# Performance work log

Measured on AMD Instinct MI355X. Metric: run time of the kernel, lower is better.

Reference implementation:

```python
import jax, jax.numpy as jnp
import numpy as np

N_HEAD = 12

def setup_inputs() -> dict:
    key = jax.random.key(0)
    k1, k2, k3 = jax.random.split(key, 3)
    B, T, C = 1, 4096, 768
    x = jax.random.normal(k1, (B, T, C), dtype=jnp.float32)
    w_attn = jax.random.normal(k2, (C, 3 * C), dtype=jnp.float32) * 0.02
    w_proj = jax.random.normal(k3, (C, C), dtype=jnp.float32) * 0.02
    return {"x": x, "w_attn": w_attn, "w_proj": w_proj}

def reference(x, w_attn, w_proj):
    B, T, C = x.shape
    H = N_HEAD
    hd = C // H
    scale = 1.0 / jnp.sqrt(jnp.asarray(hd, dtype=x.dtype))
    qkv = x @ w_attn  # [B,T,3C]
    q, k, v = jnp.split(qkv, 3, axis=-1)
    # [B,T,C] -> [B,H,T,hd]
    q = q.reshape(B, T, H, hd).transpose(0, 2, 1, 3)
    k = k.reshape(B, T, H, hd).transpose(0, 2, 1, 3)
    v = v.reshape(B, T, H, hd).transpose(0, 2, 1, 3)
    att = jnp.einsum("bhqd,bhkd->bhqk", q, k) * scale  # [B,H,T,T]
    causal = jnp.tril(jnp.ones((T, T), dtype=bool))
    att = jnp.where(causal[None, None], att, -jnp.inf)
    att = jax.nn.softmax(att, axis=-1)
    y = jnp.einsum("bhqk,bhkd->bhqd", att, v)  # [B,H,T,hd]
    y = y.transpose(0, 2, 1, 3).reshape(B, T, C)
    return y @ w_proj
```

## Files before the change

### kernel.cpp

```cpp
#include <hip/hip_runtime.h>
#include <hip/hip_bf16.h>

typedef __attribute__((ext_vector_type(8))) short bfx8;
typedef __attribute__((ext_vector_type(4))) short bfx4;
typedef __attribute__((ext_vector_type(4))) float f32x4;
typedef __attribute__((ext_vector_type(4))) unsigned int u32x4;
typedef __attribute__((ext_vector_type(2))) unsigned int u32x2;

#define T_SEQ 4096
#define C_DIM 768
#define NH    12
#define HD    64
#define QKV_N 2304
#define QK_N  1536

#define MFMA16(a, b, c) __builtin_amdgcn_mfma_f32_16x16x32_bf16((a), (b), (c), 0, 0, 0)

#if __has_builtin(__builtin_amdgcn_exp2f)
#define EXP2(x) __builtin_amdgcn_exp2f(x)
#else
#define EXP2(x) exp2f(x)
#endif

__device__ __forceinline__ short f2bf(float f) {
  __hip_bfloat16 h = __float2bfloat16(f);
  return __builtin_bit_cast(short, h);
}

__device__ __forceinline__ void pl16(unsigned& a, unsigned& b) {
#if __has_builtin(__builtin_amdgcn_permlane16_swap)
  u32x2 r = __builtin_amdgcn_permlane16_swap(a, b, false, false);
  a = r[0]; b = r[1];
#else
  unsigned ax = (unsigned)__shfl_xor((int)a, 16, 64);
  unsigned bx = (unsigned)__shfl_xor((int)b, 16, 64);
  bool odd = ((threadIdx.x >> 4) & 1) != 0;
  unsigned na = odd ? bx : a;
  unsigned nb = odd ? b : ax;
  a = na; b = nb;
#endif
}
__device__ __forceinline__ void pl32(unsigned& a, unsigned& b) {
#if __has_builtin(__builtin_amdgcn_permlane32_swap)
  u32x2 r = __builtin_amdgcn_permlane32_swap(a, b, false, false);
  a = r[0]; b = r[1];
#else
  unsigned ax = (unsigned)__shfl_xor((int)a, 32, 64);
  unsigned bx = (unsigned)__shfl_xor((int)b, 32, 64);
  bool hi = ((threadIdx.x >> 5) & 1) != 0;
  unsigned na = hi ? bx : a;
  unsigned nb = hi ? b : ax;
  a = na; b = nb;
#endif
}

__global__ __launch_bounds__(256) void conv_bf16_kernel(
    const float* __restrict__ in, short* __restrict__ out, int n4) {
  int i = blockIdx.x * 256 + threadIdx.x;
  if (i >= n4) return;
  float4 v = ((const float4*)in)[i];
  bfx4 o;
  o[0] = f2bf(v.x); o[1] = f2bf(v.y); o[2] = f2bf(v.z); o[3] = f2bf(v.w);
  ((bfx4*)out)[i] = o;
}

__global__ __launch_bounds__(256) void transpose_bf16_kernel(
    const float* __restrict__ in, short* __restrict__ out, int R, int Cc,
    int qcols, float qscale) {
  __shared__ short tile[32][33];
  int bx = blockIdx.x * 32, by = blockIdx.y * 32;
  int tx = threadIdx.x & 31, ty = threadIdx.x >> 5;
  float sc = (bx + tx) < qcols ? qscale : 1.0f;
#pragma unroll
  for (int i = 0; i < 32; i += 8)
    tile[ty + i][tx] = f2bf(in[(size_t)(by + ty + i) * Cc + (bx + tx)] * sc);
  __syncthreads();
#pragma unroll
  for (int i = 0; i < 32; i += 8)
    out[(size_t)(bx + ty + i) * R + (by + tx)] = tile[tx][ty + i];
}

template <int MODE>
__global__ __launch_bounds__(256) void gemm_bf16(
    const short* __restrict__ A, const short* __restrict__ Bt,
    void* __restrict__ Cout, short* __restrict__ Vt,
    int M, int N, int K) {
  __shared__ short As[2][128 * 32];
  __shared__ short Bs[2][128 * 32];
  const int tid  = threadIdx.x;
  const int lane = tid & 63;
  const int wave = tid >> 6;
  const int am0 = blockIdx.x * 128;
  const int bn0 = blockIdx.y * 128;
  const int wr = (wave >> 1) * 64;
  const int wc = (wave & 1) * 64;

  const int idx0 = tid,       r0 = idx0 >> 2, c0 = (idx0 & 3) * 8;
  const int idx1 = 256 + tid, r1 = idx1 >> 2, c1 = (idx1 & 3) * 8;

#define GSTAGE(buf, k0)                                                                 \
  do {                                                                                  \
    __builtin_amdgcn_global_load_lds(                                                   \
        (const __attribute__((address_space(1))) void*)(A + (size_t)(am0 + r0) * K + (k0) + c0), \
        (__attribute__((address_space(3))) void*)(&As[buf][idx0 * 8]), 16, 0, 0);       \
    __builtin_amdgcn_global_load_lds(                                                   \
        (const __attribute__((address_space(1))) void*)(A + (size_t)(am0 + r1) * K + (k0) + c1), \
        (__attribute__((address_space(3))) void*)(&As[buf][idx1 * 8]), 16, 0, 0);       \
    __builtin_amdgcn_global_load_lds(                                                   \
        (const __attribute__((address_space(1))) void*)(Bt + (size_t)(bn0 + r0) * K + (k0) + c0), \
        (__attribute__((address_space(3))) void*)(&Bs[buf][idx0 * 8]), 16, 0, 0);       \
    __builtin_amdgcn_global_load_lds(                                                   \
        (const __attribute__((address_space(1))) void*)(Bt + (size_t)(bn0 + r1) * K + (k0) + c1), \
        (__attribute__((address_space(3))) void*)(&Bs[buf][idx1 * 8]), 16, 0, 0);       \
  } while (0)

  const f32x4 zero = {0.f, 0.f, 0.f, 0.f};
  f32x4 acc[4][4];
#pragma unroll
  for (int i = 0; i < 4; i++)
#pragma unroll
    for (int j = 0; j < 4; j++) acc[i][j] = zero;

  const int aoff = (wr + (lane & 15)) * 32 + (lane >> 4) * 8;
  const int boff = (wc + (lane & 15)) * 32 + (lane >> 4) * 8;

  const int nk = K / 32;
  GSTAGE(0, 0);
  for (int t = 0; t < nk; t++) {
    const int cur = t & 1;
    if (t + 1 < nk) {
      GSTAGE(cur ^ 1, (t + 1) * 32);
      asm volatile("s_waitcnt vmcnt(4)" ::: "memory");
    } else {
      asm volatile("s_waitcnt vmcnt(0)" ::: "memory");
    }
    __builtin_amdgcn_s_barrier();

    bfx8 a[4], b[4];
#pragma unroll
    for (int mf = 0; mf < 4; mf++)
      a[mf] = *(const bfx8*)&As[cur][aoff + mf * 16 * 32];
#pragma unroll
    for (int nf = 0; nf < 4; nf++)
      b[nf] = *(const bfx8*)&Bs[cur][boff + nf * 16 * 32];
#pragma unroll
    for (int mf = 0; mf < 4; mf++)
#pragma unroll
      for (int nf = 0; nf < 4; nf++)
        acc[mf][nf] = MFMA16(a[mf], b[nf], acc[mf][nf]);

    asm volatile("s_waitcnt lgkmcnt(0)" ::: "memory");
    __builtin_amdgcn_s_barrier();
  }
#undef GSTAGE

  if (MODE == 1 && bn0 >= QK_N) {
#pragma unroll
    for (int mf = 0; mf < 4; mf++) {
      int row0 = am0 + wr + mf * 16 + (lane >> 4) * 4;
#pragma unroll
      for (int nf = 0; nf < 4; nf++) {
        int colV = bn0 - QK_N + wc + nf * 16 + (lane & 15);
        bfx4 ov;
#pragma unroll
        for (int r = 0; r < 4; r++) ov[r] = f2bf(acc[mf][nf][r]);
        *(bfx4*)&Vt[(size_t)colV * T_SEQ + row0] = ov;
      }
    }
  } else {
#pragma unroll
    for (int mf = 0; mf < 4; mf++) {
#pragma unroll
      for (int r = 0; r < 4; r++) {
        int row = am0 + wr + mf * 16 + (lane >> 4) * 4 + r;
#pragma unroll
        for (int nf = 0; nf < 4; nf++) {
          int col = bn0 + wc + nf * 16 + (lane & 15);
          float v = acc[mf][nf][r];
          if (MODE == 1)
            ((short*)Cout)[(size_t)row * QK_N + col] = f2bf(v);
          else
            ((float*)Cout)[(size_t)row * N + col] = v;
        }
      }
    }
  }
}

__global__ __launch_bounds__(256) void attn_kernel(
    const short* __restrict__ qk, const short* __restrict__ Vt,
    short* __restrict__ yb) {
  __shared__ short Ks[2][64 * 64];
  __shared__ short Vs[2][64 * 64];

  const int tid  = threadIdx.x;
  const int lane = tid & 63;
  const int wv   = tid >> 6;
  const int col  = lane & 15;
  const int g    = lane >> 4;

  const int bid = blockIdx.x;
  const int h   = bid % NH;
  const int pr  = bid / NH;
  const int myi = (wv < 2) ? (127 - pr) : pr;
  const int qw  = myi * 32 + (wv & 1) * 16;
  const int nt  = ((127 - pr) * 32 + 31) / 64 + 1;

  const int hq = h * HD;
  const int hk = C_DIM + h * HD;
  const short* Vth = Vt + (size_t)h * HD * T_SEQ;

  const int sidx0 = tid;
  const int sidx1 = 256 + tid;
  const int srow0 = sidx0 >> 3, sslot0 = (sidx0 & 7) ^ (srow0 & 7);
  const int srow1 = sidx1 >> 3, sslot1 = (sidx1 & 7) ^ (srow1 & 7);

#define STAGE(buf, kvoff)                                                               \
  do {                                                                                  \
    __builtin_amdgcn_global_load_lds(                                                   \
        (const __attribute__((address_space(1))) void*)(qk + (size_t)((kvoff) + srow0) * QK_N + hk + sslot0 * 8), \
        (__attribute__((address_space(3))) void*)(&Ks[buf][sidx0 * 8]), 16, 0, 0);      \
    __builtin_amdgcn_global_load_lds(                                                   \
        (const __attribute__((address_space(1))) void*)(qk + (size_t)((kvoff) + srow1) * QK_N + hk + sslot1 * 8), \
        (__attribute__((address_space(3))) void*)(&Ks[buf][sidx1 * 8]), 16, 0, 0);      \
    __builtin_amdgcn_global_load_lds(                                                   \
        (const __attribute__((address_space(1))) void*)(Vth + (size_t)srow0 * T_SEQ + (kvoff) + sslot0 * 8), \
        (__attribute__((address_space(3))) void*)(&Vs[buf][sidx0 * 8]), 16, 0, 0);      \
    __builtin_amdgcn_global_load_lds(                                                   \
        (const __attribute__((address_space(1))) void*)(Vth + (size_t)srow1 * T_SEQ + (kvoff) + sslot1 * 8), \
        (__attribute__((address_space(3))) void*)(&Vs[buf][sidx1 * 8]), 16, 0, 0);      \
  } while (0)

  bfx8 qf[2];
#pragma unroll
  for (int hf = 0; hf < 2; hf++)
    qf[hf] = *(const bfx8*)&qk[(size_t)(qw + col) * QK_N + hq + hf * 32 + g * 8];

  int koff[4][2], voff[2][4];
#pragma unroll
  for (int sub = 0; sub < 4; sub++) {
    int row = sub * 16 + col;
#pragma unroll
    for (int hf = 0; hf < 2; hf++)
      koff[sub][hf] = row * 64 + ((((hf << 2) | g) ^ (row & 7)) * 8);
  }
#pragma unroll
  for (int ks = 0; ks < 2; ks++)
#pragma unroll
    for (int c = 0; c < 4; c++) {
      int row = c * 16 + col;
      voff[ks][c] = row * 64 + ((((ks << 2) | g) ^ (row & 7)) * 8);
    }

  bfx8 ones;
#pragma unroll
  for (int j = 0; j < 8; j++) ones[j] = (short)0x3F80;

  const f32x4 zero = {0.f, 0.f, 0.f, 0.f};
  f32x4 o[4];
#pragma unroll
  for (int c = 0; c < 4; c++) o[c] = zero;
  f32x4 o_l = zero;

  const int qabs = qw + col;

#define TILE_BODY(BUF, KV)                                                              \
  do {                                                                                  \
    if ((KV) <= qw + 15) {                                                              \
      bfx8 kf[4][2];                                                                    \
      _Pragma("unroll") for (int sub = 0; sub < 4; sub++)                               \
          _Pragma("unroll") for (int hf = 0; hf < 2; hf++)                              \
              kf[sub][hf] = *(const bfx8*)&Ks[BUF][koff[sub][hf]];                      \
      bfx8 vtf[2][4];                                                                   \
      _Pragma("unroll") for (int ks = 0; ks < 2; ks++)                                  \
          _Pragma("unroll") for (int c = 0; c < 4; c++)                                 \
              vtf[ks][c] = *(const bfx8*)&Vs[BUF][voff[ks][c]];                         \
      f32x4 s[4];                                                                       \
      __builtin_amdgcn_s_setprio(1);                                                    \
      _Pragma("unroll") for (int sub = 0; sub < 4; sub++) {                             \
        s[sub] = zero;                                                                  \
        s[sub] = MFMA16(kf[sub][0], qf[0], s[sub]);                                     \
        s[sub] = MFMA16(kf[sub][1], qf[1], s[sub]);                                     \
      }                                                                                 \
      __builtin_amdgcn_s_setprio(0);                                                    \
      if (!((KV) + 63 <= qw)) {                                                         \
        _Pragma("unroll") for (int sub = 0; sub < 4; sub++)                             \
            _Pragma("unroll") for (int r = 0; r < 4; r++) {                             \
              int key = (KV) + sub * 16 + 4 * g + r;                                    \
              if (key > qabs) s[sub][r] = -INFINITY;                                    \
            }                                                                           \
      }                                                                                 \
      unsigned u[4][4];                                                                 \
      _Pragma("unroll") for (int sub = 0; sub < 4; sub++)                               \
          _Pragma("unroll") for (int r = 0; r < 4; r++) {                               \
            float pv = EXP2(s[sub][r]);                                                 \
            u[sub][r] = __builtin_bit_cast(unsigned, pv) & 0xFFFF0000u;                 \
          }                                                                             \
      _Pragma("unroll") for (int ks = 0; ks < 2; ks++) {                                \
        unsigned x0 = u[2 * ks][1] | (u[2 * ks][0] >> 16);                              \
        unsigned y0 = u[2 * ks + 1][1] | (u[2 * ks + 1][0] >> 16);                      \
        unsigned x1 = u[2 * ks][3] | (u[2 * ks][2] >> 16);                              \
        unsigned y1 = u[2 * ks + 1][3] | (u[2 * ks + 1][2] >> 16);                      \
        pl32(x0, y0); pl16(x0, y0);                                                     \
        pl32(x1, y1); pl16(x1, y1);                                                     \
        u32x4 w; w[0] = x0; w[1] = x1; w[2] = y0; w[3] = y1;                            \
        bfx8 pf = __builtin_bit_cast(bfx8, w);                                          \
        __builtin_amdgcn_s_setprio(1);                                                  \
        _Pragma("unroll") for (int c = 0; c < 4; c++)                                   \
            o[c] = MFMA16(vtf[ks][c], pf, o[c]);                                        \
        o_l = MFMA16(ones, pf, o_l);                                                    \
        __builtin_amdgcn_s_setprio(0);                                                  \
      }                                                                                 \
    }                                                                                   \
  } while (0)

  STAGE(0, 0);

  int t = 0;
  while (true) {
    if (t + 1 < nt) {
      STAGE(1, (t + 1) * 64);
      asm volatile("s_waitcnt vmcnt(4)" ::: "memory");
    } else {
      asm volatile("s_waitcnt vmcnt(0)" ::: "memory");
    }
    __builtin_amdgcn_s_barrier();
    TILE_BODY(0, t * 64);
    asm volatile("s_waitcnt lgkmcnt(0)" ::: "memory");
    __builtin_amdgcn_s_barrier();
    if (++t >= nt) break;

    if (t + 1 < nt) {
      STAGE(0, (t + 1) * 64);
      asm volatile("s_waitcnt vmcnt(4)" ::: "memory");
    } else {
      asm volatile("s_waitcnt vmcnt(0)" ::: "memory");
    }
    __builtin_amdgcn_s_barrier();
    TILE_BODY(1, t * 64);
    asm volatile("s_waitcnt lgkmcnt(0)" ::: "memory");
    __builtin_amdgcn_s_barrier();
    if (++t >= nt) break;
  }

  float inv = 1.f / o_l[0];
#pragma unroll
  for (int c = 0; c < 4; c++) {
    bfx4 ov;
#pragma unroll
    for (int r = 0; r < 4; r++) ov[r] = f2bf(o[c][r] * inv);
    *(bfx4*)&yb[(size_t)(qw + col) * C_DIM + h * HD + c * 16 + g * 4] = ov;
  }
#undef TILE_BODY
#undef STAGE
}

extern "C" void kernel_launch(void* const* d_in, const int* in_sizes, int n_in,
                              void* d_out, int out_size, void* d_ws, size_t ws_size,
                              hipStream_t stream) {
  const float* x      = (const float*)d_in[0];
  const float* w_attn = (const float*)d_in[1];
  const float* w_proj = (const float*)d_in[2];
  float* out = (float*)d_out;

  char* ws = (char*)d_ws;
  short* xb  = (short*)(ws);
  short* wab = (short*)(ws + 6291456);
  short* wpb = (short*)(ws + 9830400);
  short* qk  = (short*)(ws + 11010048);
  short* Vt  = (short*)(ws + 23592960);
  short* yb  = (short*)(ws + 29884416);

  conv_bf16_kernel<<<3072, 256, 0, stream>>>(x, xb, 786432);
  transpose_bf16_kernel<<<dim3(QKV_N / 32, C_DIM / 32), 256, 0, stream>>>(
      w_attn, wab, C_DIM, QKV_N, C_DIM, 0.125f * 1.4426950408889634f);
  transpose_bf16_kernel<<<dim3(C_DIM / 32, C_DIM / 32), 256, 0, stream>>>(
      w_proj, wpb, C_DIM, C_DIM, 0, 1.0f);

  gemm_bf16<1><<<dim3(T_SEQ / 128, QKV_N / 128), 256, 0, stream>>>(
      xb, wab, (void*)qk, Vt, T_SEQ, QKV_N, C_DIM);
  attn_kernel<<<64 * NH, 256, 0, stream>>>(qk, Vt, yb);
  gemm_bf16<0><<<dim3(T_SEQ / 128, C_DIM / 128), 256, 0, stream>>>(
      yb, wpb, (void*)out, nullptr, T_SEQ, C_DIM, C_DIM);
}
```

Baseline: 122.2 us.

## Process two 16-row query groups per wave in attention, halving block threads

The attention block drops from four waves to two, and each wave now handles 32 query rows (two 16-row groups) instead of 16. The K/V fragments read from LDS are reused across both groups, which halves LDS read traffic per query. Staging is redistributed so 128 threads issue four loads each. The probability packing also switches to a byte-permute helper. The cost is higher register pressure and fewer waves per block to hide latency, so occupancy or latency hiding may suffer.

```diff
diff --git a/kernel.cpp b/kernel.cpp
--- a/kernel.cpp
+++ b/kernel.cpp
@@ -25,6 +25,16 @@
 __device__ __forceinline__ short f2bf(float f) {
   __hip_bfloat16 h = __float2bfloat16(f);
   return __builtin_bit_cast(short, h);
+}
+
+__device__ __forceinline__ unsigned packtrunc(float p_even, float p_odd) {
+#if __has_builtin(__builtin_amdgcn_perm)
+  return __builtin_amdgcn_perm(__builtin_bit_cast(unsigned, p_odd),
+                               __builtin_bit_cast(unsigned, p_even), 0x07060302u);
+#else
+  return (__builtin_bit_cast(unsigned, p_odd) & 0xFFFF0000u) |
+         (__builtin_bit_cast(unsigned, p_even) >> 16);
+#endif
 }
 
 __device__ __forceinline__ void pl16(unsigned& a, unsigned& b) {
@@ -187,7 +197,7 @@
   }
 }
 
-__global__ __launch_bounds__(256) void attn_kernel(
+__global__ __launch_bounds__(128) void attn_kernel(
     const short* __restrict__ qk, const short* __restrict__ Vt,
     short* __restrict__ yb) {
   __shared__ short Ks[2][64 * 64];
@@ -202,39 +212,40 @@
   const int bid = blockIdx.x;
   const int h   = bid % NH;
   const int pr  = bid / NH;
-  const int myi = (wv < 2) ? (127 - pr) : pr;
-  const int qw  = myi * 32 + (wv & 1) * 16;
+  const int myi = (wv == 0) ? (127 - pr) : pr;
+  const int qw  = myi * 32;
   const int nt  = ((127 - pr) * 32 + 31) / 64 + 1;
 
   const int hq = h * HD;
   const int hk = C_DIM + h * HD;
   const short* Vth = Vt + (size_t)h * HD * T_SEQ;
 
-  const int sidx0 = tid;
-  const int sidx1 = 256 + tid;
-  const int srow0 = sidx0 >> 3, sslot0 = (sidx0 & 7) ^ (srow0 & 7);
-  const int srow1 = sidx1 >> 3, sslot1 = (sidx1 & 7) ^ (srow1 & 7);
+  int srow[4], sslot[4], sidx[4];
+#pragma unroll
+  for (int i = 0; i < 4; i++) {
+    sidx[i] = i * 128 + tid;
+    srow[i] = sidx[i] >> 3;
+    sslot[i] = (sidx[i] & 7) ^ (srow[i] & 7);
+  }
 
 #define STAGE(buf, kvoff)                                                               \
   do {                                                                                  \
-    __builtin_amdgcn_global_load_lds(                                                   \
-        (const __attribute__((address_space(1))) void*)(qk + (size_t)((kvoff) + srow0) * QK_N + hk + sslot0 * 8), \
-        (__attribute__((address_space(3))) void*)(&Ks[buf][sidx0 * 8]), 16, 0, 0);      \
-    __builtin_amdgcn_global_load_lds(                                                   \
-        (const __attribute__((address_space(1))) void*)(qk + (size_t)((kvoff) + srow1) * QK_N + hk + sslot1 * 8), \
-        (__attribute__((address_space(3))) void*)(&Ks[buf][sidx1 * 8]), 16, 0, 0);      \
-    __builtin_amdgcn_global_load_lds(                                                   \
-        (const __attribute__((address_space(1))) void*)(Vth + (size_t)srow0 * T_SEQ + (kvoff) + sslot0 * 8), \
-        (__attribute__((address_space(3))) void*)(&Vs[buf][sidx0 * 8]), 16, 0, 0);      \
-    __builtin_amdgcn_global_load_lds(                                                   \
-        (const __attribute__((address_space(1))) void*)(Vth + (size_t)srow1 * T_SEQ + (kvoff) + sslot1 * 8), \
-        (__attribute__((address_space(3))) void*)(&Vs[buf][sidx1 * 8]), 16, 0, 0);      \
+    _Pragma("unroll") for (int i = 0; i < 4; i++) {                                     \
+      __builtin_amdgcn_global_load_lds(                                                 \
+          (const __attribute__((address_space(1))) void*)(qk + (size_t)((kvoff) + srow[i]) * QK_N + hk + sslot[i] * 8), \
+          (__attribute__((address_space(3))) void*)(&Ks[buf][sidx[i] * 8]), 16, 0, 0);  \
+      __builtin_amdgcn_global_load_lds(                                                 \
+          (const __attribute__((address_space(1))) void*)(Vth + (size_t)srow[i] * T_SEQ + (kvoff) + sslot[i] * 8), \
+          (__attribute__((address_space(3))) void*)(&Vs[buf][sidx[i] * 8]), 16, 0, 0);  \
+    }                                                                                   \
   } while (0)
 
-  bfx8 qf[2];
-#pragma unroll
-  for (int hf = 0; hf < 2; hf++)
-    qf[hf] = *(const bfx8*)&qk[(size_t)(qw + col) * QK_N + hq + hf * 32 + g * 8];
+  bfx8 qf[2][2];
+#pragma unroll
+  for (int qq = 0; qq < 2; qq++)
+#pragma unroll
+    for (int hf = 0; hf < 2; hf++)
+      qf[qq][hf] = *(const bfx8*)&qk[(size_t)(qw + qq * 16 + col) * QK_N + hq + hf * 32 + g * 8];
 
   int koff[4][2], voff[2][4];
 #pragma unroll
@@ -257,16 +268,16 @@
   for (int j = 0; j < 8; j++) ones[j] = (short)0x3F80;
 
   const f32x4 zero = {0.f, 0.f, 0.f, 0.f};
-  f32x4 o[4];
-#pragma unroll
-  for (int c = 0; c < 4; c++) o[c] = zero;
-  f32x4 o_l = zero;
-
-  const int qabs = qw + col;
+  f32x4 o[2][4];
+#pragma unroll
+  for (int qq = 0; qq < 2; qq++)
+#pragma unroll
+    for (int c = 0; c < 4; c++) o[qq][c] = zero;
+  f32x4 ol[2] = {zero, zero};
 
 #define TILE_BODY(BUF, KV)                                                              \
   do {                                                                                  \
-    if ((KV) <= qw + 15) {                                                              \
+    if ((KV) <= qw + 31) {                                                              \
       bfx8 kf[4][2];                                                                    \
       _Pragma("unroll") for (int sub = 0; sub < 4; sub++)                               \
           _Pragma("unroll") for (int hf = 0; hf < 2; hf++)                              \
@@ -275,41 +286,46 @@
       _Pragma("unroll") for (int ks = 0; ks < 2; ks++)                                  \
           _Pragma("unroll") for (int c = 0; c < 4; c++)                                 \
               vtf[ks][c] = *(const bfx8*)&Vs[BUF][voff[ks][c]];                         \
-      f32x4 s[4];                                                                       \
+      f32x4 s[2][4];                                                                    \
       __builtin_amdgcn_s_setprio(1);                                                    \
-      _Pragma("unroll") for (int sub = 0; sub < 4; sub++) {                             \
-        s[sub] = zero;                                                                  \
-        s[sub] = MFMA16(kf[sub][0], qf[0], s[sub]);                                     \
-        s[sub] = MFMA16(kf[sub][1], qf[1], s[sub]);                                     \
-      }                                                                                 \
+      _Pragma("unroll") for (int qq = 0; qq < 2; qq++)                                  \
+          _Pragma("unroll") for (int sub = 0; sub < 4; sub++) {                         \
+            s[qq][sub] = zero;                                                          \
+            s[qq][sub] = MFMA16(kf[sub][0], qf[qq][0], s[qq][sub]);                     \
+            s[qq][sub] = MFMA16(kf[sub][1], qf[qq][1], s[qq][sub]);                     \
+          }                                                                             \
       __builtin_amdgcn_s_setprio(0);                                                    \
       if (!((KV) + 63 <= qw)) {                                                         \
-        _Pragma("unroll") for (int sub = 0; sub < 4; sub++)                             \
-            _Pragma("unroll") for (int r = 0; r < 4; r++) {                             \
-              int key = (KV) + sub * 16 + 4 * g + r;                                    \
-              if (key > qabs) s[sub][r] = -INFINITY;                                    \
-            }                                                                           \
+        _Pragma("unroll") for (int qq = 0; qq < 2; qq++) {                              \
+          int qabs = qw + qq * 16 + col;                                                \
+          _Pragma("unroll") for (int sub = 0; sub < 4; sub++)                           \
+              _Pragma("unroll") for (int r = 0; r < 4; r++) {                           \
+                int key = (KV) + sub * 16 + 4 * g + r;                                  \
+                if (key > qabs) s[qq][sub][r] = -INFINITY;                              \
+              }                                                                         \
+        }                                                                               \
       }                                                                                 \
-      unsigned u[4][4];                                                                 \
-      _Pragma("unroll") for (int sub = 0; sub < 4; sub++)                               \
-          _Pragma("unroll") for (int r = 0; r < 4; r++) {                               \
-            float pv = EXP2(s[sub][r]);                                                 \
-            u[sub][r] = __builtin_bit_cast(unsigned, pv) & 0xFFFF0000u;                 \
-          }                                                                             \
+      float p[2][4][4];                                                                 \
+      _Pragma("unroll") for (int qq = 0; qq < 2; qq++)                                  \
+          _Pragma("unroll") for (int sub = 0; sub < 4; sub++)                           \
+              _Pragma("unroll") for (int r = 0; r < 4; r++)                             \
+                  p[qq][sub][r] = EXP2(s[qq][sub][r]);                                  \
       _Pragma("unroll") for (int ks = 0; ks < 2; ks++) {                                \
-        unsigned x0 = u[2 * ks][1] | (u[2 * ks][0] >> 16);                              \
-        unsigned y0 = u[2 * ks + 1][1] | (u[2 * ks + 1][0] >> 16);                      \
-        unsigned x1 = u[2 * ks][3] | (u[2 * ks][2] >> 16);                              \
-        unsigned y1 = u[2 * ks + 1][3] | (u[2 * ks + 1][2] >> 16);                      \
-        pl32(x0, y0); pl16(x0, y0);                                                     \
-        pl32(x1, y1); pl16(x1, y1);                                                     \
-        u32x4 w; w[0] = x0; w[1] = x1; w[2] = y0; w[3] = y1;                            \
-        bfx8 pf = __builtin_bit_cast(bfx8, w);                                          \
-        __builtin_amdgcn_s_setprio(1);                                                  \
-        _Pragma("unroll") for (int c = 0; c < 4; c++)                                   \
-            o[c] = MFMA16(vtf[ks][c], pf, o[c]);                                        \
-        o_l = MFMA16(ones, pf, o_l);                                                    \
-        __builtin_amdgcn_s_setprio(0);                                                  \
+        _Pragma("unroll") for (int qq = 0; qq < 2; qq++) {                              \
+          unsigned x0 = packtrunc(p[qq][2 * ks][0], p[qq][2 * ks][1]);                  \
+          unsigned y0 = packtrunc(p[qq][2 * ks + 1][0], p[qq][2 * ks + 1][1]);          \
+          unsigned x1 = packtrunc(p[qq][2 * ks][2], p[qq][2 * ks][3]);                  \
+          unsigned y1 = packtrunc(p[qq][2 * ks + 1][2], p[qq][2 * ks + 1][3]);          \
+          pl32(x0, y0); pl16(x0, y0);                                                   \
+          pl32(x1, y1); pl16(x1, y1);                                                   \
+          u32x4 w; w[0] = x0; w[1] = x1; w[2] = y0; w[3] = y1;                          \
+          bfx8 pf = __builtin_bit_cast(bfx8, w);                                        \
+          __builtin_amdgcn_s_setprio(1);                                                \
+          _Pragma("unroll") for (int c = 0; c < 4; c++)                                 \
+              o[qq][c] = MFMA16(vtf[ks][c], pf, o[qq][c]);                              \
+          ol[qq] = MFMA16(ones, pf, ol[qq]);                                            \
+          __builtin_amdgcn_s_setprio(0);                                                \
+        }                                                                               \
       }                                                                                 \
     }                                                                                   \
   } while (0)
@@ -320,7 +336,7 @@
   while (true) {
     if (t + 1 < nt) {
       STAGE(1, (t + 1) * 64);
-      asm volatile("s_waitcnt vmcnt(4)" ::: "memory");
+      asm volatile("s_waitcnt vmcnt(8)" ::: "memory");
     } else {
       asm volatile("s_waitcnt vmcnt(0)" ::: "memory");
     }
@@ -332,7 +348,7 @@
 
     if (t + 1 < nt) {
       STAGE(0, (t + 1) * 64);
-      asm volatile("s_waitcnt vmcnt(4)" ::: "memory");
+      asm volatile("s_waitcnt vmcnt(8)" ::: "memory");
     } else {
       asm volatile("s_waitcnt vmcnt(0)" ::: "memory");
     }
@@ -343,13 +359,16 @@
     if (++t >= nt) break;
   }
 
-  float inv = 1.f / o_l[0];
-#pragma unroll
-  for (int c = 0; c < 4; c++) {
-    bfx4 ov;
-#pragma unroll
-    for (int r = 0; r < 4; r++) ov[r] = f2bf(o[c][r] * inv);
-    *(bfx4*)&yb[(size_t)(qw + col) * C_DIM + h * HD + c * 16 + g * 4] = ov;
+#pragma unroll
+  for (int qq = 0; qq < 2; qq++) {
+    float inv = 1.f / ol[qq][0];
+#pragma unroll
+    for (int c = 0; c < 4; c++) {
+      bfx4 ov;
+#pragma unroll
+      for (int r = 0; r < 4; r++) ov[r] = f2bf(o[qq][c][r] * inv);
+      *(bfx4*)&yb[(size_t)(qw + qq * 16 + col) * C_DIM + h * HD + c * 16 + g * 4] = ov;
+    }
   }
 #undef TILE_BODY
 #undef STAGE
@@ -379,7 +398,7 @@
 
   gemm_bf16<1><<<dim3(T_SEQ / 128, QKV_N / 128), 256, 0, stream>>>(
       xb, wab, (void*)qk, Vt, T_SEQ, QKV_N, C_DIM);
-  attn_kernel<<<64 * NH, 256, 0, stream>>>(qk, Vt, yb);
+  attn_kernel<<<64 * NH, 128, 0, stream>>>(qk, Vt, yb);
   gemm_bf16<0><<<dim3(T_SEQ / 128, C_DIM / 128), 256, 0, stream>>>(
       yb, wpb, (void*)out, nullptr, T_SEQ, C_DIM, C_DIM);
 }
```

Measured after the change: 136.3 us. 1.12x slower.

## Merge prep kernels into one launch and retile projection GEMM to 64x64

Applied to the files above, without the earlier changes.

The fp32-to-bf16 conversion of x and the two weight transposes now run in a single prep kernel, dispatched by block index, instead of three launches. The output projection GEMM gets its own kernel with 64x64 tiles, giving 768 blocks instead of 192 so the GPU's compute units are better covered. The aim is to cut launch overhead and the under-filled GPU in the final GEMM. In exchange, the smaller tiles reuse less data per block from LDS and global memory.

```diff
diff --git a/kernel.cpp b/kernel.cpp
--- a/kernel.cpp
+++ b/kernel.cpp
@@ -54,37 +54,49 @@
 #endif
 }
 
-__global__ __launch_bounds__(256) void conv_bf16_kernel(
-    const float* __restrict__ in, short* __restrict__ out, int n4) {
-  int i = blockIdx.x * 256 + threadIdx.x;
-  if (i >= n4) return;
-  float4 v = ((const float4*)in)[i];
-  bfx4 o;
-  o[0] = f2bf(v.x); o[1] = f2bf(v.y); o[2] = f2bf(v.z); o[3] = f2bf(v.w);
-  ((bfx4*)out)[i] = o;
-}
-
-__global__ __launch_bounds__(256) void transpose_bf16_kernel(
-    const float* __restrict__ in, short* __restrict__ out, int R, int Cc,
-    int qcols, float qscale) {
+#define NB_CONV 3072
+#define NB_TA   (72 * 24)
+#define NB_TB   (24 * 24)
+__global__ __launch_bounds__(256) void prep_kernel(
+    const float* __restrict__ x, short* __restrict__ xb,
+    const float* __restrict__ w_attn, short* __restrict__ wab,
+    const float* __restrict__ w_proj, short* __restrict__ wpb) {
   __shared__ short tile[32][33];
-  int bx = blockIdx.x * 32, by = blockIdx.y * 32;
+  const int b = blockIdx.x;
+  if (b < NB_CONV) {
+    int i = b * 256 + threadIdx.x;
+    float4 v = ((const float4*)x)[i];
+    bfx4 o;
+    o[0] = f2bf(v.x); o[1] = f2bf(v.y); o[2] = f2bf(v.z); o[3] = f2bf(v.w);
+    ((bfx4*)xb)[i] = o;
+    return;
+  }
+  const float* in; short* out; int Cc, bx, by, qcols;
+  if (b < NB_CONV + NB_TA) {
+    int bb = b - NB_CONV;
+    in = w_attn; out = wab; Cc = QKV_N;
+    bx = (bb % 72) * 32; by = (bb / 72) * 32;
+    qcols = C_DIM;
+  } else {
+    int bb = b - NB_CONV - NB_TA;
+    in = w_proj; out = wpb; Cc = C_DIM;
+    bx = (bb % 24) * 32; by = (bb / 24) * 32;
+    qcols = 0;
+  }
   int tx = threadIdx.x & 31, ty = threadIdx.x >> 5;
-  float sc = (bx + tx) < qcols ? qscale : 1.0f;
+  float sc = (bx + tx) < qcols ? 0.125f * 1.4426950408889634f : 1.0f;
 #pragma unroll
   for (int i = 0; i < 32; i += 8)
     tile[ty + i][tx] = f2bf(in[(size_t)(by + ty + i) * Cc + (bx + tx)] * sc);
   __syncthreads();
 #pragma unroll
   for (int i = 0; i < 32; i += 8)
-    out[(size_t)(bx + ty + i) * R + (by + tx)] = tile[tx][ty + i];
-}
-
-template <int MODE>
-__global__ __launch_bounds__(256) void gemm_bf16(
+    out[(size_t)(bx + ty + i) * C_DIM + (by + tx)] = tile[tx][ty + i];
+}
+
+__global__ __launch_bounds__(256) void gemm_qkv(
     const short* __restrict__ A, const short* __restrict__ Bt,
-    void* __restrict__ Cout, short* __restrict__ Vt,
-    int M, int N, int K) {
+    short* __restrict__ qk, short* __restrict__ Vt, int K) {
   __shared__ short As[2][128 * 32];
   __shared__ short Bs[2][128 * 32];
   const int tid  = threadIdx.x;
@@ -154,7 +166,7 @@
   }
 #undef GSTAGE
 
-  if (MODE == 1 && bn0 >= QK_N) {
+  if (bn0 >= QK_N) {
 #pragma unroll
     for (int mf = 0; mf < 4; mf++) {
       int row0 = am0 + wr + mf * 16 + (lane >> 4) * 4;
@@ -176,12 +188,87 @@
 #pragma unroll
         for (int nf = 0; nf < 4; nf++) {
           int col = bn0 + wc + nf * 16 + (lane & 15);
-          float v = acc[mf][nf][r];
-          if (MODE == 1)
-            ((short*)Cout)[(size_t)row * QK_N + col] = f2bf(v);
-          else
-            ((float*)Cout)[(size_t)row * N + col] = v;
+          qk[(size_t)row * QK_N + col] = f2bf(acc[mf][nf][r]);
         }
+      }
+    }
+  }
+}
+
+__global__ __launch_bounds__(256) void gemm_proj(
+    const short* __restrict__ A, const short* __restrict__ Bt,
+    float* __restrict__ C, int N, int K) {
+  __shared__ short As[2][64 * 32];
+  __shared__ short Bs[2][64 * 32];
+  const int tid  = threadIdx.x;
+  const int lane = tid & 63;
+  const int wave = tid >> 6;
+  const int am0 = blockIdx.x * 64;
+  const int bn0 = blockIdx.y * 64;
+  const int wr = (wave >> 1) * 32;
+  const int wc = (wave & 1) * 32;
+
+  const int r0 = tid >> 2, c0 = (tid & 3) * 8;
+
+#define PSTAGE(buf, k0)                                                                 \
+  do {                                                                                  \
+    __builtin_amdgcn_global_load_lds(                                                   \
+        (const __attribute__((address_space(1))) void*)(A + (size_t)(am0 + r0) * K + (k0) + c0), \
+        (__attribute__((address_space(3))) void*)(&As[buf][tid * 8]), 16, 0, 0);        \
+    __builtin_amdgcn_global_load_lds(                                                   \
+        (const __attribute__((address_space(1))) void*)(Bt + (size_t)(bn0 + r0) * K + (k0) + c0), \
+        (__attribute__((address_space(3))) void*)(&Bs[buf][tid * 8]), 16, 0, 0);        \
+  } while (0)
+
+  const f32x4 zero = {0.f, 0.f, 0.f, 0.f};
+  f32x4 acc[2][2];
+#pragma unroll
+  for (int i = 0; i < 2; i++)
+#pragma unroll
+    for (int j = 0; j < 2; j++) acc[i][j] = zero;
+
+  const int aoff = (wr + (lane & 15)) * 32 + (lane >> 4) * 8;
+  const int boff = (wc + (lane & 15)) * 32 + (lane >> 4) * 8;
+
+  const int nk = K / 32;
+  PSTAGE(0, 0);
+  for (int t = 0; t < nk; t++) {
+    const int cur = t & 1;
+    if (t + 1 < nk) {
+      PSTAGE(cur ^ 1, (t + 1) * 32);
+      asm volatile("s_waitcnt vmcnt(2)" ::: "memory");
+    } else {
+      asm volatile("s_waitcnt vmcnt(0)" ::: "memory");
+    }
+    __builtin_amdgcn_s_barrier();
+
+    bfx8 a[2], b[2];
+#pragma unroll
+    for (int mf = 0; mf < 2; mf++)
+      a[mf] = *(const bfx8*)&As[cur][aoff + mf * 16 * 32];
+#pragma unroll
+    for (int nf = 0; nf < 2; nf++)
+      b[nf] = *(const bfx8*)&Bs[cur][boff + nf * 16 * 32];
+#pragma unroll
+    for (int mf = 0; mf < 2; mf++)
+#pragma unroll
+      for (int nf = 0; nf < 2; nf++)
+        acc[mf][nf] = MFMA16(a[mf], b[nf], acc[mf][nf]);
+
+    asm volatile("s_waitcnt lgkmcnt(0)" ::: "memory");
+    __builtin_amdgcn_s_barrier();
+  }
+#undef PSTAGE
+
+#pragma unroll
+  for (int mf = 0; mf < 2; mf++) {
+#pragma unroll
+    for (int r = 0; r < 4; r++) {
+      int row = am0 + wr + mf * 16 + (lane >> 4) * 4 + r;
+#pragma unroll
+      for (int nf = 0; nf < 2; nf++) {
+        int col = bn0 + wc + nf * 16 + (lane & 15);
+        C[(size_t)row * N + col] = acc[mf][nf][r];
       }
     }
   }
@@ -371,15 +458,8 @@
   short* Vt  = (short*)(ws + 23592960);
   short* yb  = (short*)(ws + 29884416);
 
-  conv_bf16_kernel<<<3072, 256, 0, stream>>>(x, xb, 786432);
-  transpose_bf16_kernel<<<dim3(QKV_N / 32, C_DIM / 32), 256, 0, stream>>>(
-      w_attn, wab, C_DIM, QKV_N, C_DIM, 0.125f * 1.4426950408889634f);
-  transpose_bf16_kernel<<<dim3(C_DIM / 32, C_DIM / 32), 256, 0, stream>>>(
-      w_proj, wpb, C_DIM, C_DIM, 0, 1.0f);
-
-  gemm_bf16<1><<<dim3(T_SEQ / 128, QKV_N / 128), 256, 0, stream>>>(
-      xb, wab, (void*)qk, Vt, T_SEQ, QKV_N, C_DIM);
+  prep_kernel<<<NB_CONV + NB_TA + NB_TB, 256, 0, stream>>>(x, xb, w_attn, wab, w_proj, wpb);
+  gemm_qkv<<<dim3(T_SEQ / 128, QKV_N / 128), 256, 0, stream>>>(xb, wab, qk, Vt, C_DIM);
   attn_kernel<<<64 * NH, 256, 0, stream>>>(qk, Vt, yb);
-  gemm_bf16<0><<<dim3(T_SEQ / 128, C_DIM / 128), 256, 0, stream>>>(
-      yb, wpb, (void*)out, nullptr, T_SEQ, C_DIM, C_DIM);
-}
+  gemm_proj<<<dim3(T_SEQ / 64, C_DIM / 64), 256, 0, stream>>>(yb, wpb, out, C_DIM, C_DIM);
+}
```

Result: faster. 112.6 us (-7.8%).
